# Kernel tuning notes

Measured on AMD Instinct MI355X. Metric: run time of the kernel, lower is better.

The kernel has to match this reference:

```python
import jax, jax.numpy as jnp
import numpy as np

# ---- static config (mirrors VectorQuantizer2.__init__) ----
V_PATCH = [1, 2, 3, 4, 6, 9, 13, 18, 24, 32]
SN = len(V_PATCH)
BETA = 0.25
QRESI = 0.5                      # Phi.resi_ratio = |quant_resi|
K_PHI = 4                        # share_quant_resi (PhiPartiallyShared)
TICKS = np.linspace(1.0 / 3 / K_PHI, 1.0 - 1.0 / 3 / K_PHI, K_PHI)  # K==4 branch
_A = -0.75                       # torch bicubic kernel coefficient


def _cubic(x):
    x = np.abs(x)
    return np.where(x <= 1.0, ((_A + 2.0) * x - (_A + 3.0)) * x * x + 1.0,
           np.where(x < 2.0, _A * (((x - 5.0) * x + 8.0) * x - 4.0), 0.0))


def _resize_mat(n_in, n_out, align_corners):
    # [n_out, n_in] separable torch-bicubic interpolation matrix (border-replicated)
    M = np.zeros((n_out, n_in), np.float32)
    for o in range(n_out):
        if align_corners:
            src = 0.0 if n_out == 1 else o * (n_in - 1) / (n_out - 1)
        else:
            src = (o + 0.5) * n_in / n_out - 0.5
        fl = int(np.floor(src)); t = src - fl
        for k in range(-1, 3):
            M[o, min(max(fl + k, 0), n_in - 1)] += float(_cubic(k - t))
    return jnp.asarray(M)


def _resize(x, hw, align_corners):
    # x: [B,C,H,W] -> [B,C,hw[0],hw[1]], bicubic, separable matmuls
    Mh = _resize_mat(x.shape[2], hw[0], align_corners)
    Mw = _resize_mat(x.shape[3], hw[1], align_corners)
    return jnp.einsum('oh,pw,bchw->bcop', Mh, Mw, x)


def _phi(h, w, b, r):
    # Phi: h*(1-r) + Conv3x3(h)*r
    y = jax.lax.conv_general_dilated(h, w, (1, 1), 'SAME',
                                     dimension_numbers=('NCHW', 'OIHW', 'NCHW'))
    y = y + b[None, :, None, None]
    return h * (1.0 - r) + y * r


def setup_inputs() -> dict:
    key = jax.random.key(0)
    k1, k2, k3 = jax.random.split(key, 3)
    B, C, H, W, V = 1024, 64, 32, 1, 4096
    f = jax.random.normal(k1, (B, C, H, W), jnp.float32)
    emb_weight = jax.random.normal(k2, (V, C), jnp.float32) * 0.02
    phi_w = jax.random.normal(k3, (K_PHI, C, C, 3, 3), jnp.float32) / np.sqrt(C * 9.0)
    phi_b = jnp.zeros((K_PHI, C), jnp.float32)
    return {"f_BChw": f, "emb_weight": emb_weight, "phi_w": phi_w, "phi_b": phi_b}


def reference(f_BChw, emb_weight, phi_w, phi_b):
    f = f_BChw.astype(jnp.float32)
    B, C, H, W = f.shape
    f_ng = jax.lax.stop_gradient(f)
    f_rest = f_ng
    f_hat = jnp.zeros_like(f_ng)
    e_ng = jax.lax.stop_gradient(emb_weight)
    e_sq = jnp.sum(e_ng * e_ng, axis=1)          # [V]
    loss = jnp.float32(0.0)
    levels = []
    for si, pn in enumerate(V_PATCH):
        ph, pw = pn, 1
        if si != SN - 1:
            rest = _resize(f_rest, (ph, pw), align_corners=True)
        else:
            rest = f                                  # last scale quantizes f itself
        rest_NC = jax.lax.stop_gradient(rest.transpose(0, 2, 3, 1).reshape(-1, C))
        d = jnp.sum(rest_NC * rest_NC, axis=1, keepdims=True) + e_sq \
            - 2.0 * (rest_NC @ e_ng.T)                # [N, V] squared distances
        idx = jnp.argmin(d, axis=1)                   # [N]
        h = emb_weight[idx.reshape(B, ph, pw)].transpose(0, 3, 1, 2)  # [B,C,ph,pw]
        if si != SN - 1:
            h = _resize(h, (H, W), align_corners=False)
        pi = int(np.argmin(np.abs(TICKS - si / (SN - 1))))
        h = _phi(h, phi_w[pi], phi_b[pi], QRESI)
        f_hat = f_hat + h
        f_rest = f_rest - h
        loss = loss + BETA * jnp.mean((jax.lax.stop_gradient(f_hat) - f) ** 2) \
                    + jnp.mean((f_hat - f_ng) ** 2)
        levels.append(f_hat)
    loss = loss / SN
    f_hat_st = jax.lax.stop_gradient(f_hat) - f_ng + f   # straight-through
    return f_hat_st, loss, jnp.stack(levels)
```

## Files before the change

kernel.cpp:

```cpp
#include <hip/hip_runtime.h>
#include <math.h>

#define BB 1024
#define CC 64
#define HH 32
#define VV 4096
#define NEL (BB*CC*HH)

#define RT 128

typedef __attribute__((ext_vector_type(4))) float f32x4;
typedef __attribute__((ext_vector_type(8))) short bf16x8;


__device__ double dev_cubic(double x){
#pragma clang fp contract(off)
  const double A = -0.75;
  x = fabs(x);
  if (x <= 1.0) return ((A + 2.0)*x - (A + 3.0))*x*x + 1.0;
  if (x < 2.0)  return A*(((x - 5.0)*x + 8.0)*x - 4.0);
  return 0.0;
}

__device__ __constant__ int c_vpatch[10] = {1,2,3,4,6,9,13,18,24,32};
__device__ __constant__ int c_pref[10]   = {0,1,3,6,10,16,25,38,56,80};

__global__ void gen_setup(float* Mdown, float* Mup, double* partial){
#pragma clang fp contract(off)
  int t = threadIdx.x;
  for (int i = t; i < 3584; i += 64) { Mdown[i] = 0.0f; Mup[i] = 0.0f; }
  if (t < 16) partial[t] = 0.0;
  __syncthreads();
  if (t < 20) {
    int si = t >> 1; int up = t & 1;
    int pn = c_vpatch[si];
    if (!up) {
      float* M = Mdown + c_pref[si]*32;
      for (int o = 0; o < pn; o++){
        double src = (pn == 1) ? 0.0 : (double)(o*(32-1)) / (double)(pn-1);
        double fl = floor(src); double tt = src - fl; int fli = (int)fl;
        for (int k = -1; k <= 2; k++){
          int j = fli + k; j = j < 0 ? 0 : (j > 31 ? 31 : j);
          float w = (float)dev_cubic((double)k - tt);
          M[o*32 + j] = M[o*32 + j] + w;
        }
      }
    } else {
      float* M = Mup + c_pref[si]*32;
      for (int o = 0; o < 32; o++){
        double src = ((double)o + 0.5) * (double)pn / 32.0 - 0.5;
        double fl = floor(src); double tt = src - fl; int fli = (int)fl;
        for (int k = -1; k <= 2; k++){
          int j = fli + k; j = j < 0 ? 0 : (j > pn-1 ? pn-1 : j);
          float w = (float)dev_cubic((double)k - tt);
          M[o*pn + j] = M[o*pn + j] + w;
        }
      }
    }
  }
}

__global__ void pack_w(const float* __restrict__ w, float* __restrict__ wPack){
  for (int e = blockIdx.x*blockDim.x + threadIdx.x; e < 4*64*196; e += gridDim.x*blockDim.x){
    int pi = e / (64*196);
    int r  = e - pi*64*196;
    int co = r / 196, m = r - co*196;
    float v = 0.0f;
    if (m < 192){
      int ci = m / 3, kh = m - ci*3;
      v = w[(((pi*64 + co)*64 + ci)*3 + kh)*3 + 1];
    }
    wPack[e] = v;
  }
}

__device__ float np_pairwise8_sq64(const float* a){
#pragma clang fp contract(off)
  float r0 = a[0]*a[0], r1 = a[1]*a[1], r2 = a[2]*a[2], r3 = a[3]*a[3];
  float r4 = a[4]*a[4], r5 = a[5]*a[5], r6 = a[6]*a[6], r7 = a[7]*a[7];
  for (int i = 8; i < 64; i += 8){
    float s0 = a[i+0]*a[i+0]; r0 = r0 + s0;
    float s1 = a[i+1]*a[i+1]; r1 = r1 + s1;
    float s2 = a[i+2]*a[i+2]; r2 = r2 + s2;
    float s3 = a[i+3]*a[i+3]; r3 = r3 + s3;
    float s4 = a[i+4]*a[i+4]; r4 = r4 + s4;
    float s5 = a[i+5]*a[i+5]; r5 = r5 + s5;
    float s6 = a[i+6]*a[i+6]; r6 = r6 + s6;
    float s7 = a[i+7]*a[i+7]; r7 = r7 + s7;
  }
  return ((r0 + r1) + (r2 + r3)) + ((r4 + r5) + (r6 + r7));
}

__device__ inline void split3t(float a, unsigned short& s1, unsigned short& s2, unsigned short& s3){
  unsigned u1 = __float_as_uint(a);
  s1 = (unsigned short)(u1 >> 16);
  float f1 = __uint_as_float(u1 & 0xffff0000u);
  float r1 = a - f1;
  unsigned u2 = __float_as_uint(r1);
  s2 = (unsigned short)(u2 >> 16);
  float f2 = __uint_as_float(u2 & 0xffff0000u);
  float r2 = r1 - f2;
  s3 = (unsigned short)(__float_as_uint(r2) >> 16);
}
__device__ inline float bf_up(short h){
  return __uint_as_float(((unsigned)(unsigned short)h) << 16);
}

__global__ void prep_emb(const float* __restrict__ emb, unsigned short* __restrict__ ePack,
                         float* __restrict__ e_sq){
#pragma clang fp contract(off)
  int v = blockIdx.x*blockDim.x + threadIdx.x;
  if (v >= VV) return;
  float row[64];
  for (int c = 0; c < CC; c++) row[c] = emb[v*CC + c];
  e_sq[v] = np_pairwise8_sq64(row);
  int vt = v >> 4, col = v & 15;
  for (int c = 0; c < CC; c++){
    unsigned short s1, s2, s3;
    split3t(row[c], s1, s2, s3);
    int kk = c >> 5, g = (c >> 3) & 3, jj = c & 7;
    size_t base = ((size_t)((vt*2 + kk)*3))*512 + (size_t)(g*16 + col)*8 + jj;
    ePack[base       ] = s1;
    ePack[base +  512] = s2;
    ePack[base + 1024] = s3;
  }
}

__global__ __launch_bounds__(256) void init_k(const float* __restrict__ f,
    float* frest, float* fhat, float* rest0, const float* Md0){
#pragma clang fp contract(off)
  __shared__ float frL[64][33];
  __shared__ float m0[32];
  int b = blockIdx.x, t = threadIdx.x;
  if (t < 32) m0[t] = Md0[t];
  for (int e = t; e < 2048; e += 256){
    int c = e >> 5, h = e & 31;
    float v = f[b*2048 + e];
    frL[c][h] = v;
    frest[b*2048 + e] = v;
    fhat[b*2048 + e] = 0.0f;
  }
  __syncthreads();
  if (t < 64){
    float s = 0.0f;
    for (int h = 0; h < 32; h++){ float pr = m0[h]*frL[t][h]; s = s + pr; }
    rest0[b*64 + t] = s;
  }
}


template<int PN, int NSPLIT>
__global__ __launch_bounds__(256,3) void argmin_mfma(const float* __restrict__ rest,
    const unsigned short* __restrict__ ePack, const float* __restrict__ e_sq,
    float* __restrict__ bestW, int* __restrict__ idxW)
{
#pragma clang fp contract(off)
  constexpr int VSPL = VV / NSPLIT;
  constexpr int NVT  = VSPL / 16;
  constexpr int CH   = 4;
  constexpr int NR   = NVT / CH;
  static_assert(NVT % CH == 0, "NVT must be multiple of CH");

  __shared__ __align__(16) union {
    unsigned short rP[3*8192];
    unsigned short eS[2][CH*6*512];
  } u;
  __shared__ float sR[RT];
  __shared__ float esL[VSPL];

  const int n0    = blockIdx.x * RT;
  const int split = blockIdx.y;
  const int v0    = split * VSPL;
  const int t     = threadIdx.x;
  const int lane  = t & 63;
  const int w     = t >> 6;

  const unsigned short* gW = ePack + (size_t)(v0 >> 4)*3072
                           + (size_t)w*6*512 + (size_t)lane*8;
  bf16x8 st[6];
#pragma unroll
  for (int c = 0; c < 6; c++) st[c] = *(const bf16x8*)(gW + c*512);

  {
    int j  = t & 127;
    int o0 = t >> 7;
    int nrow = n0 + j;
    int b = nrow / PN, p = nrow % PN;
    int rt_ = j >> 4, m = j & 15;
#pragma unroll
    for (int i = 0; i < 4; i++){
      int o  = o0 + 2*i;
      int kk = o >> 2, g = o & 3;
      bf16x8 v1, v2, v3;
#pragma unroll
      for (int cc = 0; cc < 8; cc++){
        float a = rest[((size_t)b*CC + (o*8 + cc))*PN + p];
        unsigned short s1, s2, s3;
        split3t(a, s1, s2, s3);
        v1[cc] = (short)s1; v2[cc] = (short)s2; v3[cc] = (short)s3;
      }
      int eb = ((rt_*2 + kk)*64 + g*16 + m)*8;
      *(bf16x8*)&u.rP[eb        ] = v1;
      *(bf16x8*)&u.rP[eb +  8192] = v2;
      *(bf16x8*)&u.rP[eb + 16384] = v3;
    }
    for (int e = t; e < VSPL; e += 256) esL[e] = e_sq[v0 + e];
  }
  __syncthreads();

  if (t < RT){
    int rt_ = t >> 4, m = t & 15;
    float q[8];
#pragma unroll
    for (int o = 0; o < 8; o++){
      int kk = o >> 2, g = o & 3;
      int eb = ((rt_*2 + kk)*64 + g*16 + m)*8;
      bf16x8 h1 = *(const bf16x8*)&u.rP[eb        ];
      bf16x8 h2 = *(const bf16x8*)&u.rP[eb +  8192];
      bf16x8 h3 = *(const bf16x8*)&u.rP[eb + 16384];
#pragma unroll
      for (int cc = 0; cc < 8; cc++){
        float a = (bf_up(h1[cc]) + bf_up(h2[cc])) + bf_up(h3[cc]);
        float s = a*a;
        if (o == 0) q[cc] = s; else q[cc] = q[cc] + s;
      }
    }
    sR[t] = ((q[0] + q[1]) + (q[2] + q[3])) + ((q[4] + q[5]) + (q[6] + q[7]));
  }

  bf16x8 aF[2][2][3];
  const int rt0 = w*2;
#pragma unroll
  for (int r2 = 0; r2 < 2; r2++)
#pragma unroll
    for (int kk = 0; kk < 2; kk++)
#pragma unroll
      for (int sp = 0; sp < 3; sp++)
        aF[r2][kk][sp] = *(const bf16x8*)&u.rP[sp*8192 + (((rt0+r2)*2 + kk)*64 + lane)*8];
  __syncthreads();

#pragma unroll
  for (int c = 0; c < 6; c++)
    *(bf16x8*)&u.eS[0][(w*6 + c)*512 + (size_t)lane*8] = st[c];
  __syncthreads();

  f32x4 sRl[2];
  sRl[0] = *(const f32x4*)&sR[(rt0+0)*16 + (lane>>4)*4];
  sRl[1] = *(const f32x4*)&sR[(rt0+1)*16 + (lane>>4)*4];

  float best[2][4]; int bidx[2][4];
#pragma unroll
  for (int r2 = 0; r2 < 2; r2++)
#pragma unroll
    for (int rg = 0; rg < 4; rg++){ best[r2][rg] = 3.0e38f; bidx[r2][rg] = 0; }

#define CTILE(eF, VT) do { \
    f32x4 acc0 = {0.f,0.f,0.f,0.f}; \
    f32x4 acc1 = {0.f,0.f,0.f,0.f}; \
    acc0 = __builtin_amdgcn_mfma_f32_16x16x32_bf16(aF[0][0][0], eF[0], acc0, 0,0,0); \
    acc1 = __builtin_amdgcn_mfma_f32_16x16x32_bf16(aF[1][0][0], eF[0], acc1, 0,0,0); \
    acc0 = __builtin_amdgcn_mfma_f32_16x16x32_bf16(aF[0][0][0], eF[1], acc0, 0,0,0); \
    acc1 = __builtin_amdgcn_mfma_f32_16x16x32_bf16(aF[1][0][0], eF[1], acc1, 0,0,0); \
    acc0 = __builtin_amdgcn_mfma_f32_16x16x32_bf16(aF[0][0][1], eF[0], acc0, 0,0,0); \
    acc1 = __builtin_amdgcn_mfma_f32_16x16x32_bf16(aF[1][0][1], eF[0], acc1, 0,0,0); \
    acc0 = __builtin_amdgcn_mfma_f32_16x16x32_bf16(aF[0][0][1], eF[1], acc0, 0,0,0); \
    acc1 = __builtin_amdgcn_mfma_f32_16x16x32_bf16(aF[1][0][1], eF[1], acc1, 0,0,0); \
    acc0 = __builtin_amdgcn_mfma_f32_16x16x32_bf16(aF[0][0][0], eF[2], acc0, 0,0,0); \
    acc1 = __builtin_amdgcn_mfma_f32_16x16x32_bf16(aF[1][0][0], eF[2], acc1, 0,0,0); \
    acc0 = __builtin_amdgcn_mfma_f32_16x16x32_bf16(aF[0][0][2], eF[0], acc0, 0,0,0); \
    acc1 = __builtin_amdgcn_mfma_f32_16x16x32_bf16(aF[1][0][2], eF[0], acc1, 0,0,0); \
    acc0 = __builtin_amdgcn_mfma_f32_16x16x32_bf16(aF[0][1][0], eF[3], acc0, 0,0,0); \
    acc1 = __builtin_amdgcn_mfma_f32_16x16x32_bf16(aF[1][1][0], eF[3], acc1, 0,0,0); \
    acc0 = __builtin_amdgcn_mfma_f32_16x16x32_bf16(aF[0][1][0], eF[4], acc0, 0,0,0); \
    acc1 = __builtin_amdgcn_mfma_f32_16x16x32_bf16(aF[1][1][0], eF[4], acc1, 0,0,0); \
    acc0 = __builtin_amdgcn_mfma_f32_16x16x32_bf16(aF[0][1][1], eF[3], acc0, 0,0,0); \
    acc1 = __builtin_amdgcn_mfma_f32_16x16x32_bf16(aF[1][1][1], eF[3], acc1, 0,0,0); \
    acc0 = __builtin_amdgcn_mfma_f32_16x16x32_bf16(aF[0][1][1], eF[4], acc0, 0,0,0); \
    acc1 = __builtin_amdgcn_mfma_f32_16x16x32_bf16(aF[1][1][1], eF[4], acc1, 0,0,0); \
    acc0 = __builtin_amdgcn_mfma_f32_16x16x32_bf16(aF[0][1][0], eF[5], acc0, 0,0,0); \
    acc1 = __builtin_amdgcn_mfma_f32_16x16x32_bf16(aF[1][1][0], eF[5], acc1, 0,0,0); \
    acc0 = __builtin_amdgcn_mfma_f32_16x16x32_bf16(aF[0][1][2], eF[3], acc0, 0,0,0); \
    acc1 = __builtin_amdgcn_mfma_f32_16x16x32_bf16(aF[1][1][2], eF[3], acc1, 0,0,0); \
    int vt_ = (VT); \
    float es = esL[vt_*16 + (lane & 15)]; \
    int codeBase = v0 + vt_*16 + (lane & 15); \
    _Pragma("unroll") \
    for (int rg = 0; rg < 4; rg++){ \
      float t1a = sRl[0][rg] + es;                  \
      float da  = fmaf(-2.0f, acc0[rg], t1a);       \
      if (da < best[0][rg]) { best[0][rg] = da; bidx[0][rg] = codeBase; } \
      float t1b = sRl[1][rg] + es; \
      float db  = fmaf(-2.0f, acc1[rg], t1b); \
      if (db < best[1][rg]) { best[1][rg] = db; bidx[1][rg] = codeBase; } \
    } } while(0)

  int cur = 0;
  for (int r = 0; r < NR; r++){
    if (r + 1 < NR){
      const unsigned short* gR = gW + (size_t)(r+1)*24*512;
#pragma unroll
      for (int c = 0; c < 6; c++) st[c] = *(const bf16x8*)(gR + c*512);
    }
#pragma unroll
    for (int q = 0; q < CH; q++){
      bf16x8 eF[6];
#pragma unroll
      for (int k = 0; k < 6; k++)
        eF[k] = *(const bf16x8*)&u.eS[cur][(q*6 + k)*512 + (size_t)lane*8];
      CTILE(eF, r*CH + q);
    }
    if (r + 1 < NR){
#pragma unroll
      for (int c = 0; c < 6; c++)
        *(bf16x8*)&u.eS[cur ^ 1][(w*6 + c)*512 + (size_t)lane*8] = st[c];
    }
    __syncthreads();
    cur ^= 1;
  }
#undef CTILE

#pragma unroll
  for (int r2 = 0; r2 < 2; r2++)
#pragma unroll
    for (int rg = 0; rg < 4; rg++){
      float v = best[r2][rg]; int ix = bidx[r2][rg];
      for (int off = 8; off; off >>= 1){
        float ov = __shfl_down(v, off, 16);
        int   oi = __shfl_down(ix, off, 16);
        if (ov < v || (ov == v && oi < ix)) { v = ov; ix = oi; }
      }
      if ((lane & 15) == 0){
        int n = n0 + (rt0 + r2)*16 + (lane>>4)*4 + rg;
        bestW[n*NSPLIT + split] = v;
        idxW [n*NSPLIT + split] = ix;
      }
    }
}


template<int PN, int PN2, int NSPLIT, bool LAST>
__global__ __launch_bounds__(256) void fused_phi(
    const float* __restrict__ emb,
    const float* __restrict__ bestW, const int* __restrict__ idxW,
    const float* __restrict__ Mup, const float* __restrict__ wP,
    const float* __restrict__ bias, const float* __restrict__ f,
    float* fhat, float* frest, float* levels_out, float* final_out,
    float* rest_next, const float* __restrict__ Mdown_next,
    double* partial, int si)
{
#pragma clang fp contract(off)
  __shared__ float huP[64][36];
  __shared__ union { float hE[24*64]; float frL[64*33]; } u;
  __shared__ float wL[64*196];
  __shared__ float mUp[32*25];
  __shared__ float mDn[32*33];
  __shared__ int idxL[32];
  __shared__ double red[4];
  int b = blockIdx.x, t = threadIdx.x;

  if (t < PN){
    int base = (b*PN + t)*NSPLIT;
    float v = bestW[base]; int ix = idxW[base];
#pragma unroll
    for (int s = 1; s < NSPLIT; s++){
      float ov = bestW[base + s];
      if (ov < v) { v = ov; ix = idxW[base + s]; }
    }
    idxL[t] = ix;
  }
  if (t < 64){ huP[t][0] = 0.0f; huP[t][33] = 0.0f; huP[t][34] = 0.0f; huP[t][35] = 0.0f; }
  for (int e = t; e < 3136; e += 256)
    *(float4*)&wL[e*4] = *(const float4*)&wP[e*4];
  if (PN2 > 0){
    for (int e = t; e < PN2*32; e += 256){
      int p = e >> 5, h = e & 31;
      mDn[p*33 + h] = Mdown_next[e];
    }
  }
  if (!LAST){
    for (int e = t; e < 32*PN; e += 256){
      int o = e / PN, p = e - o*PN;
      mUp[o*(PN+1) + p] = Mup[e];
    }
  }
  __syncthreads();

  if (!LAST){
    for (int e = t; e < PN*64; e += 256){
      int p = e >> 6, c = e & 63;
      u.hE[p*64 + c] = emb[idxL[p]*64 + c];
    }
    __syncthreads();
    for (int e = t; e < 2048; e += 256){
      int c = e >> 5, o = e & 31;
      const float* mr = &mUp[o*(PN+1)];
      float s = 0.0f;
#pragma unroll
      for (int p = 0; p < PN; p++){ float pr = mr[p]*u.hE[p*64 + c]; s = s + pr; }
      huP[c][1 + o] = s;
    }
  } else {
    for (int e = t; e < 2048; e += 256){
      int h = e >> 6, c = e & 63;
      huP[c][1 + h] = emb[idxL[h]*64 + c];
    }
  }
  __syncthreads();

  int co = t >> 2, h0 = (t & 3) * 8;
  float y[8];
#pragma unroll
  for (int uu = 0; uu < 8; uu++) y[uu] = 0.0f;
  for (int ci4 = 0; ci4 < 64; ci4 += 4){
    float4 wa = *(const float4*)&wL[co*196 + ci4*3];
    float4 wb = *(const float4*)&wL[co*196 + ci4*3 + 4];
    float4 wc = *(const float4*)&wL[co*196 + ci4*3 + 8];
    float wv[12] = {wa.x,wa.y,wa.z,wa.w, wb.x,wb.y,wb.z,wb.w, wc.x,wc.y,wc.z,wc.w};
#pragma unroll
    for (int q = 0; q < 4; q++){
      int ci = ci4 + q;
      float4 xa = *(const float4*)&huP[ci][h0];
      float4 xb = *(const float4*)&huP[ci][h0 + 4];
      float2 xc = *(const float2*)&huP[ci][h0 + 8];
      float x[10] = {xa.x,xa.y,xa.z,xa.w, xb.x,xb.y,xb.z,xb.w, xc.x,xc.y};
      float w0 = wv[q*3], w1 = wv[q*3+1], w2 = wv[q*3+2];
#pragma unroll
      for (int uu = 0; uu < 8; uu++){
        y[uu] = fmaf(w0, x[uu],   y[uu]);
        y[uu] = fmaf(w1, x[uu+1], y[uu]);
        y[uu] = fmaf(w2, x[uu+2], y[uu]);
      }
    }
  }

  float bb = bias[co];
  double lsum = 0.0;
  int base = b*2048 + co*32 + h0;
#pragma unroll
  for (int uu = 0; uu < 8; uu++){
    float yv = y[uu] + bb;
    float hp = 0.5f*huP[co][1 + h0 + uu] + 0.5f*yv;
    float fh = fhat[base+uu] + hp;
    fhat[base+uu] = fh;
    float fr = frest[base+uu] - hp;
    frest[base+uu] = fr;
    u.frL[co*33 + h0 + uu] = fr;
    float fv = f[base+uu];
    float dv = fh - fv;
    lsum += (double)dv*(double)dv;
    levels_out[base+uu] = fh;
    if (LAST) final_out[base+uu] = dv + fv;
  }
  for (int off = 32; off; off >>= 1) lsum += __shfl_down(lsum, off);
  if ((t & 63) == 0) red[t >> 6] = lsum;
  __syncthreads();

  if (PN2 > 0){
    for (int e = t; e < 64*PN2; e += 256){
      int c = e / PN2, p = e - c*PN2;
      const float* mr = &mDn[p*33];
      float s = 0.0f;
#pragma unroll
      for (int h = 0; h < 32; h++){ float pr = mr[h]*u.frL[c*33 + h]; s = s + pr; }
      rest_next[(b*64 + c)*PN2 + p] = s;
    }
  }
  if (t == 0) atomicAdd(&partial[si], red[0] + red[1] + red[2] + red[3]);
}

__global__ void finalize(const double* partial, float* out_loss){
#pragma clang fp contract(off)
  float L = 0.0f;
  for (int si = 0; si < 10; si++){
    float m = (float)(partial[si] / (double)NEL);
    float t1 = 0.25f * m;
    L = L + t1;
    L = L + m;
  }
  L = L / 10.0f;
  *out_loss = L;
}


struct Ptrs {
  const float *f, *emb;
  unsigned short *ePack;
  float *e_sq, *frest, *fhat, *rest, *Mdown, *Mup, *wPack, *bestW;
  int *idxW;
  double *partial;
  float *out0, *out_levels;
  const float *phi_b;
};

template<int PN, int PN2, int NSPLIT, bool LAST>
static void run_scale(const Ptrs& P, int si, int pi, int mup_off, int mdn_off,
                      hipStream_t stream){
  constexpr int N = BB*PN;
  dim3 ag(N/RT, NSPLIT);
  const float* restp = LAST ? P.f : P.rest;
  argmin_mfma<PN, NSPLIT><<<ag, 256, 0, stream>>>(restp, P.ePack, P.e_sq, P.bestW, P.idxW);
  fused_phi<PN, PN2, NSPLIT, LAST><<<BB, 256, 0, stream>>>(
      P.emb, P.bestW, P.idxW, P.Mup + mup_off,
      P.wPack + (size_t)pi*64*196, P.phi_b + (size_t)pi*CC,
      P.f, P.fhat, P.frest, P.out_levels + (size_t)si*NEL, P.out0,
      P.rest, P.Mdown + mdn_off, P.partial, si);
}

extern "C" void kernel_launch(void* const* d_in, const int* in_sizes, int n_in,
                              void* d_out, int out_size, void* d_ws, size_t ws_size,
                              hipStream_t stream) {
  const float* f     = (const float*)d_in[0];
  const float* emb   = (const float*)d_in[1];
  const float* phi_w = (const float*)d_in[2];
  const float* phi_b = (const float*)d_in[3];
  float* out0       = (float*)d_out;
  float* out_loss   = out0 + NEL;
  float* out_levels = out0 + NEL + 1;

  double* partial      = (double*)d_ws;
  unsigned short* ePack = (unsigned short*)(partial + 16);
  float*  e_sq    = (float*)(ePack + 786432 + 4096);
  float*  frest   = e_sq + 4096;
  float*  fhat    = frest + NEL;
  float*  rest    = fhat + NEL;
  float*  Mdown   = rest + NEL;
  float*  Mup     = Mdown + 3584;
  float*  wPack   = Mup + 3584;
  float*  bestW   = wPack + 50176;
  int*    idxW    = (int*)(bestW + 262144);

  double q = 1.0/3.0; q = q/4.0;
  double start = q;
  double stop  = 1.0 - q;
  double delta = stop - start;
  double step  = delta/3.0;
  double ticks[4];
  ticks[0] = start;
  ticks[1] = step + start;
  { double t2 = 2.0*step; ticks[2] = t2 + start; }
  ticks[3] = stop;
  int pi_tab[10];
  for (int si = 0; si < 10; si++){
    double x = (double)si / 9.0;
    int bi = 0; double bd = fabs(ticks[0] - x);
    for (int i2 = 1; i2 < 4; i2++){
      double dd = fabs(ticks[i2] - x);
      if (dd < bd) { bd = dd; bi = i2; }
    }
    pi_tab[si] = bi;
  }

  static const int pref[10] = {0,1,3,6,10,16,25,38,56,80};

  gen_setup<<<1, 64, 0, stream>>>(Mdown, Mup, partial);
  pack_w<<<64, 256, 0, stream>>>(phi_w, wPack);
  prep_emb<<<16, 256, 0, stream>>>(emb, ePack, e_sq);
  init_k<<<BB, 256, 0, stream>>>(f, frest, fhat, rest, Mdown );

  Ptrs P = {f, emb, ePack, e_sq, frest, fhat, rest, Mdown, Mup, wPack, bestW,
            idxW, partial, out0, out_levels, phi_b};

  run_scale< 1,  2, 32, false>(P, 0, pi_tab[0], pref[0]*32, pref[1]*32, stream);
  run_scale< 2,  3, 32, false>(P, 1, pi_tab[1], pref[1]*32, pref[2]*32, stream);
  run_scale< 3,  4, 32, false>(P, 2, pi_tab[2], pref[2]*32, pref[3]*32, stream);
  run_scale< 4,  6, 32, false>(P, 3, pi_tab[3], pref[3]*32, pref[4]*32, stream);
  run_scale< 6,  9, 16, false>(P, 4, pi_tab[4], pref[4]*32, pref[5]*32, stream);
  run_scale< 9, 13, 16, false>(P, 5, pi_tab[5], pref[5]*32, pref[6]*32, stream);
  run_scale<13, 18,  8, false>(P, 6, pi_tab[6], pref[6]*32, pref[7]*32, stream);
  run_scale<18, 24,  8, false>(P, 7, pi_tab[7], pref[7]*32, pref[8]*32, stream);
  run_scale<24,  0,  8, false>(P, 8, pi_tab[8], pref[8]*32, 0,          stream);
  run_scale<32,  0,  8, true >(P, 9, pi_tab[9], pref[9]*32, 0,          stream);

  finalize<<<1, 1, 0, stream>>>(partial, out_loss);
}
```

Measured before the change: 1.125 ms.

## Load residual fragments directly to registers and shrink LDS staging for higher occupancy

```diff
diff --git a/kernel.cpp b/kernel.cpp
--- a/kernel.cpp
+++ b/kernel.cpp
@@ -150,23 +150,20 @@
 
 
 template<int PN, int NSPLIT>
-__global__ __launch_bounds__(256,3) void argmin_mfma(const float* __restrict__ rest,
+__global__ __launch_bounds__(256,4) void argmin_mfma(const float* __restrict__ rest,
     const unsigned short* __restrict__ ePack, const float* __restrict__ e_sq,
     float* __restrict__ bestW, int* __restrict__ idxW)
 {
 #pragma clang fp contract(off)
   constexpr int VSPL = VV / NSPLIT;
   constexpr int NVT  = VSPL / 16;
-  constexpr int CH   = 4;
+  constexpr int CH   = 2;
   constexpr int NR   = NVT / CH;
   static_assert(NVT % CH == 0, "NVT must be multiple of CH");
 
-  __shared__ __align__(16) union {
-    unsigned short rP[3*8192];
-    unsigned short eS[2][CH*6*512];
-  } u;
+  __shared__ __align__(16) unsigned short eS[2][CH*6*512];
+  __shared__ float esL[VSPL];
   __shared__ float sR[RT];
-  __shared__ float esL[VSPL];
 
   const int n0    = blockIdx.x * RT;
   const int split = blockIdx.y;
@@ -174,79 +171,72 @@
   const int t     = threadIdx.x;
   const int lane  = t & 63;
   const int w     = t >> 6;
+  const int m     = lane & 15;
+  const int g     = lane >> 4;
 
   const unsigned short* gW = ePack + (size_t)(v0 >> 4)*3072
-                           + (size_t)w*6*512 + (size_t)lane*8;
-  bf16x8 st[6];
-#pragma unroll
-  for (int c = 0; c < 6; c++) st[c] = *(const bf16x8*)(gW + c*512);
-
-  {
-    int j  = t & 127;
-    int o0 = t >> 7;
-    int nrow = n0 + j;
-    int b = nrow / PN, p = nrow % PN;
-    int rt_ = j >> 4, m = j & 15;
-#pragma unroll
-    for (int i = 0; i < 4; i++){
-      int o  = o0 + 2*i;
-      int kk = o >> 2, g = o & 3;
-      bf16x8 v1, v2, v3;
-#pragma unroll
-      for (int cc = 0; cc < 8; cc++){
-        float a = rest[((size_t)b*CC + (o*8 + cc))*PN + p];
+                           + (size_t)w*3*512 + (size_t)lane*8;
+  bf16x8 st[3];
+#pragma unroll
+  for (int c = 0; c < 3; c++) st[c] = *(const bf16x8*)(gW + c*512);
+
+  for (int e = t; e < VSPL; e += 256) esL[e] = e_sq[v0 + e];
+
+  bf16x8 aF[2][2][3];
+  const int rt0 = w*2;
+#pragma unroll
+  for (int r2 = 0; r2 < 2; r2++){
+    int n = n0 + (rt0 + r2)*16 + m;
+    int b = n / PN, p = n % PN;
+    const float* rb = rest + (size_t)b*CC*PN + p;
+#pragma unroll
+    for (int kk = 0; kk < 2; kk++){
+#pragma unroll
+      for (int jj = 0; jj < 8; jj++){
+        int c = kk*32 + g*8 + jj;
+        float a = rb[(size_t)c*PN];
         unsigned short s1, s2, s3;
         split3t(a, s1, s2, s3);
-        v1[cc] = (short)s1; v2[cc] = (short)s2; v3[cc] = (short)s3;
+        aF[r2][kk][0][jj] = (short)s1;
+        aF[r2][kk][1][jj] = (short)s2;
+        aF[r2][kk][2][jj] = (short)s3;
       }
-      int eb = ((rt_*2 + kk)*64 + g*16 + m)*8;
-      *(bf16x8*)&u.rP[eb        ] = v1;
-      *(bf16x8*)&u.rP[eb +  8192] = v2;
-      *(bf16x8*)&u.rP[eb + 16384] = v3;
-    }
-    for (int e = t; e < VSPL; e += 256) esL[e] = e_sq[v0 + e];
-  }
+    }
+  }
+
+  if (t < RT){
+    int n = n0 + t;
+    int b = n / PN, p = n % PN;
+    const float* rb = rest + (size_t)b*CC*PN + p;
+    float a0 = rb[0];              float r0 = a0*a0;
+    float a1 = rb[(size_t)1*PN];   float r1 = a1*a1;
+    float a2 = rb[(size_t)2*PN];   float r2 = a2*a2;
+    float a3 = rb[(size_t)3*PN];   float r3 = a3*a3;
+    float a4 = rb[(size_t)4*PN];   float r4 = a4*a4;
+    float a5 = rb[(size_t)5*PN];   float r5 = a5*a5;
+    float a6 = rb[(size_t)6*PN];   float r6 = a6*a6;
+    float a7 = rb[(size_t)7*PN];   float r7 = a7*a7;
+    for (int i = 8; i < 64; i += 8){
+      float b0 = rb[(size_t)(i+0)*PN]; float s0 = b0*b0; r0 = r0 + s0;
+      float b1 = rb[(size_t)(i+1)*PN]; float s1 = b1*b1; r1 = r1 + s1;
+      float b2 = rb[(size_t)(i+2)*PN]; float s2 = b2*b2; r2 = r2 + s2;
+      float b3 = rb[(size_t)(i+3)*PN]; float s3 = b3*b3; r3 = r3 + s3;
+      float b4 = rb[(size_t)(i+4)*PN]; float s4 = b4*b4; r4 = r4 + s4;
+      float b5 = rb[(size_t)(i+5)*PN]; float s5 = b5*b5; r5 = r5 + s5;
+      float b6 = rb[(size_t)(i+6)*PN]; float s6 = b6*b6; r6 = r6 + s6;
+      float b7 = rb[(size_t)(i+7)*PN]; float s7 = b7*b7; r7 = r7 + s7;
+    }
+    sR[t] = ((r0 + r1) + (r2 + r3)) + ((r4 + r5) + (r6 + r7));
+  }
+
+#pragma unroll
+  for (int c = 0; c < 3; c++)
+    *(bf16x8*)&eS[0][(w*3 + c)*512 + (size_t)lane*8] = st[c];
   __syncthreads();
 
-  if (t < RT){
-    int rt_ = t >> 4, m = t & 15;
-    float q[8];
-#pragma unroll
-    for (int o = 0; o < 8; o++){
-      int kk = o >> 2, g = o & 3;
-      int eb = ((rt_*2 + kk)*64 + g*16 + m)*8;
-      bf16x8 h1 = *(const bf16x8*)&u.rP[eb        ];
-      bf16x8 h2 = *(const bf16x8*)&u.rP[eb +  8192];
-      bf16x8 h3 = *(const bf16x8*)&u.rP[eb + 16384];
-#pragma unroll
-      for (int cc = 0; cc < 8; cc++){
-        float a = (bf_up(h1[cc]) + bf_up(h2[cc])) + bf_up(h3[cc]);
-        float s = a*a;
-        if (o == 0) q[cc] = s; else q[cc] = q[cc] + s;
-      }
-    }
-    sR[t] = ((q[0] + q[1]) + (q[2] + q[3])) + ((q[4] + q[5]) + (q[6] + q[7]));
-  }
-
-  bf16x8 aF[2][2][3];
-  const int rt0 = w*2;
-#pragma unroll
-  for (int r2 = 0; r2 < 2; r2++)
-#pragma unroll
-    for (int kk = 0; kk < 2; kk++)
-#pragma unroll
-      for (int sp = 0; sp < 3; sp++)
-        aF[r2][kk][sp] = *(const bf16x8*)&u.rP[sp*8192 + (((rt0+r2)*2 + kk)*64 + lane)*8];
-  __syncthreads();
-
-#pragma unroll
-  for (int c = 0; c < 6; c++)
-    *(bf16x8*)&u.eS[0][(w*6 + c)*512 + (size_t)lane*8] = st[c];
-  __syncthreads();
-
   f32x4 sRl[2];
-  sRl[0] = *(const f32x4*)&sR[(rt0+0)*16 + (lane>>4)*4];
-  sRl[1] = *(const f32x4*)&sR[(rt0+1)*16 + (lane>>4)*4];
+  sRl[0] = *(const f32x4*)&sR[(rt0+0)*16 + g*4];
+  sRl[1] = *(const f32x4*)&sR[(rt0+1)*16 + g*4];
 
   float best[2][4]; int bidx[2][4];
 #pragma unroll
@@ -257,6 +247,7 @@
 #define CTILE(eF, VT) do { \
     f32x4 acc0 = {0.f,0.f,0.f,0.f}; \
     f32x4 acc1 = {0.f,0.f,0.f,0.f}; \
+    __builtin_amdgcn_s_setprio(1); \
     acc0 = __builtin_amdgcn_mfma_f32_16x16x32_bf16(aF[0][0][0], eF[0], acc0, 0,0,0); \
     acc1 = __builtin_amdgcn_mfma_f32_16x16x32_bf16(aF[1][0][0], eF[0], acc1, 0,0,0); \
     acc0 = __builtin_amdgcn_mfma_f32_16x16x32_bf16(aF[0][0][0], eF[1], acc0, 0,0,0); \
@@ -281,9 +272,10 @@
     acc1 = __builtin_amdgcn_mfma_f32_16x16x32_bf16(aF[1][1][0], eF[5], acc1, 0,0,0); \
     acc0 = __builtin_amdgcn_mfma_f32_16x16x32_bf16(aF[0][1][2], eF[3], acc0, 0,0,0); \
     acc1 = __builtin_amdgcn_mfma_f32_16x16x32_bf16(aF[1][1][2], eF[3], acc1, 0,0,0); \
+    __builtin_amdgcn_s_setprio(0); \
     int vt_ = (VT); \
-    float es = esL[vt_*16 + (lane & 15)]; \
-    int codeBase = v0 + vt_*16 + (lane & 15); \
+    float es = esL[vt_*16 + m]; \
+    int codeBase = v0 + vt_*16 + m; \
     _Pragma("unroll") \
     for (int rg = 0; rg < 4; rg++){ \
       float t1a = sRl[0][rg] + es;                  \
@@ -297,22 +289,22 @@
   int cur = 0;
   for (int r = 0; r < NR; r++){
     if (r + 1 < NR){
-      const unsigned short* gR = gW + (size_t)(r+1)*24*512;
-#pragma unroll
-      for (int c = 0; c < 6; c++) st[c] = *(const bf16x8*)(gR + c*512);
+      const unsigned short* gR = gW + (size_t)(r+1)*CH*6*512;
+#pragma unroll
+      for (int c = 0; c < 3; c++) st[c] = *(const bf16x8*)(gR + c*512);
     }
 #pragma unroll
     for (int q = 0; q < CH; q++){
       bf16x8 eF[6];
 #pragma unroll
       for (int k = 0; k < 6; k++)
-        eF[k] = *(const bf16x8*)&u.eS[cur][(q*6 + k)*512 + (size_t)lane*8];
+        eF[k] = *(const bf16x8*)&eS[cur][(q*6 + k)*512 + (size_t)lane*8];
       CTILE(eF, r*CH + q);
     }
     if (r + 1 < NR){
 #pragma unroll
-      for (int c = 0; c < 6; c++)
-        *(bf16x8*)&u.eS[cur ^ 1][(w*6 + c)*512 + (size_t)lane*8] = st[c];
+      for (int c = 0; c < 3; c++)
+        *(bf16x8*)&eS[cur ^ 1][(w*3 + c)*512 + (size_t)lane*8] = st[c];
     }
     __syncthreads();
     cur ^= 1;
```

Result: slower. 1.273 ms (+13.1%).
